# Optimization experiments

Hardware: AMD Instinct MI355X
Metric: run time of the kernel (lower is better)

Reference implementation:

```python
import jax, jax.numpy as jnp
import numpy as np

N_PATCHES = 14
HIDDEN_D = 768
N_HEADS = 12
D_HEAD = HIDDEN_D // N_HEADS
SEQ = N_PATCHES ** 2 + 1  # 197
INPUT_D = 3 * 16 * 16  # c * patch_h * patch_w = 768
LN_EPS = 1e-5


def positional_embeddings(seq_len, d):
    # result[i, j] = sin(i / 10000**(j/d)) if j even else cos(i / 10000**((j-1)/d))
    i = jnp.arange(seq_len, dtype=jnp.float32)[:, None]
    j = jnp.arange(d, dtype=jnp.float32)[None, :]
    even = (jnp.arange(d) % 2 == 0)[None, :]
    denom_even = jnp.power(10000.0, j / d)
    denom_odd = jnp.power(10000.0, (j - 1.0) / d)
    return jnp.where(even, jnp.sin(i / denom_even), jnp.cos(i / denom_odd))


def setup_inputs() -> dict:
    key = jax.random.key(0)
    ks = jax.random.split(key, 12)
    s = 0.02
    return {
        "images": jax.random.normal(ks[0], (128, 3, 224, 224), dtype=jnp.float32),
        "W_map": jax.random.normal(ks[1], (HIDDEN_D, INPUT_D), dtype=jnp.float32) * s,
        "b_map": jax.random.normal(ks[2], (HIDDEN_D,), dtype=jnp.float32) * s,
        "class_token": jax.random.uniform(ks[3], (1, HIDDEN_D), dtype=jnp.float32),
        "ln_w": jnp.ones((SEQ, HIDDEN_D), dtype=jnp.float32),
        "ln_b": jnp.zeros((SEQ, HIDDEN_D), dtype=jnp.float32),
        "Wq": jax.random.normal(ks[4], (N_HEADS, D_HEAD, D_HEAD), dtype=jnp.float32) * s,
        "bq": jax.random.normal(ks[5], (N_HEADS, D_HEAD), dtype=jnp.float32) * s,
        "Wk": jax.random.normal(ks[6], (N_HEADS, D_HEAD, D_HEAD), dtype=jnp.float32) * s,
        "bk": jax.random.normal(ks[7], (N_HEADS, D_HEAD), dtype=jnp.float32) * s,
        "Wv": jax.random.normal(ks[8], (N_HEADS, D_HEAD, D_HEAD), dtype=jnp.float32) * s,
        "bv": jax.random.normal(ks[9], (N_HEADS, D_HEAD), dtype=jnp.float32) * s,
    }


def _forward(images, W_map, b_map, class_token, ln_w, ln_b, Wq, bq, Wk, bk, Wv, bv):
    n = images.shape[0]
    # naive patchify (faithful to source: a plain reshape)
    patches = images.reshape(n, N_PATCHES ** 2, INPUT_D)
    # linear mapper: x @ W.T + b
    tokens = jnp.einsum("npi,di->npd", patches, W_map) + b_map
    # prepend class token
    cls = jnp.broadcast_to(class_token[None], (n, 1, HIDDEN_D))
    tokens = jnp.concatenate([cls, tokens], axis=1)  # [n, SEQ, D]
    # positional embeddings
    tokens = tokens + positional_embeddings(SEQ, HIDDEN_D)[None]
    # LayerNorm over last two dims (SEQ, D) jointly
    mean = jnp.mean(tokens, axis=(-2, -1), keepdims=True)
    var = jnp.var(tokens, axis=(-2, -1), keepdims=True)
    x = (tokens - mean) / jnp.sqrt(var + LN_EPS) * ln_w + ln_b
    # multi-head self-attention (batched over samples and heads)
    xh = x.reshape(n, SEQ, N_HEADS, D_HEAD)  # head-sliced channels
    q = jnp.einsum("bshd,hed->bshe", xh, Wq) + bq[None, None]
    k = jnp.einsum("bshd,hed->bshe", xh, Wk) + bk[None, None]
    v = jnp.einsum("bshd,hed->bshe", xh, Wv) + bv[None, None]
    att = jax.nn.softmax(
        jnp.einsum("bshd,bthd->bhst", q, k) / jnp.sqrt(jnp.float32(D_HEAD)), axis=-1
    )
    msa = jnp.einsum("bhst,bthd->bshd", att, v).reshape(n, SEQ, HIDDEN_D)
    return tokens + msa


def reference(images, W_map, b_map, class_token, ln_w, ln_b, Wq, bq, Wk, bk, Wv, bv):
    return _forward(images, W_map, b_map, class_token, ln_w, ln_b, Wq, bq, Wk, bk, Wv, bv)
```

## Files before the change

kernel.cpp:

```cpp
#include <hip/hip_runtime.h>

typedef float fx4 __attribute__((ext_vector_type(4)));
typedef __bf16 bf16x8 __attribute__((ext_vector_type(8)));
typedef unsigned short ushort8 __attribute__((ext_vector_type(8)));
typedef unsigned int uint2v __attribute__((ext_vector_type(2)));
typedef unsigned int uint4v __attribute__((ext_vector_type(4)));

#define MFMA16(a, b, c) __builtin_amdgcn_mfma_f32_16x16x32_bf16((a), (b), (c), 0, 0, 0)

#if __has_builtin(__builtin_amdgcn_exp2f)
#define EXP2(x) __builtin_amdgcn_exp2f(x)
#else
#define EXP2(x) exp2f(x)
#endif

__device__ __forceinline__ unsigned short f2bf(float f) {
  return __builtin_bit_cast(unsigned short, (__bf16)f);
}

__device__ __forceinline__ ushort8 pack8(fx4 a, fx4 b) {
  ushort8 v;
  v[0] = f2bf(a[0]); v[1] = f2bf(a[1]); v[2] = f2bf(a[2]); v[3] = f2bf(a[3]);
  v[4] = f2bf(b[0]); v[5] = f2bf(b[1]); v[6] = f2bf(b[2]); v[7] = f2bf(b[3]);
  return v;
}

__device__ __forceinline__ uint2v pack2(fx4 v) {
  uint2v r;
  r[0] = (unsigned int)f2bf(v[0]) | ((unsigned int)f2bf(v[1]) << 16);
  r[1] = (unsigned int)f2bf(v[2]) | ((unsigned int)f2bf(v[3]) << 16);
  return r;
}

__device__ __forceinline__ bf16x8 xfrm(uint2v A, uint2v B, int quad, int src0, int src1) {
  uint4v pf;
#pragma unroll
  for (int d = 0; d < 2; d++) {
    int a0 = __shfl((int)A[d], src0, 64);
    int b0 = __shfl((int)B[d], src0, 64);
    pf[d] = (unsigned int)((quad < 2) ? a0 : b0);
    int a1 = __shfl((int)A[d], src1, 64);
    int b1 = __shfl((int)B[d], src1, 64);
    pf[2 + d] = (unsigned int)((quad < 2) ? a1 : b1);
  }
  return __builtin_bit_cast(bf16x8, pf);
}

__device__ __forceinline__ void gl2lds16(const unsigned short* g, void* lds_base) {
  __builtin_amdgcn_global_load_lds(
      (const __attribute__((address_space(1))) void*)(unsigned long long)(g),
      (__attribute__((address_space(3))) void*)(unsigned int)(unsigned long long)(lds_base),
      16, 0, 0);
}

__global__ __launch_bounds__(256) void k_prep(
    const float* __restrict__ img, const float* __restrict__ W,
    const float* __restrict__ Wq, const float* __restrict__ Wk, const float* __restrict__ Wv,
    const float* __restrict__ ct,
    float* __restrict__ pe, unsigned short* __restrict__ imgbf, unsigned short* __restrict__ wbf,
    unsigned short* __restrict__ wqkv,
    float* __restrict__ out, float* __restrict__ sums, float* __restrict__ sqs) {
  const int bid = blockIdx.x, tid = threadIdx.x;
  if (bid < 591) {
    int idx = bid * 256 + tid;
    int s = idx / 768;
    int j = idx - s * 768;
    int jj = j & ~1;
    float ang = (float)s * expf((float)jj * (-9.210340371976184f / 768.0f));
    pe[idx] = (j & 1) ? cosf(ang) : sinf(ang);
  } else if (bid < 10287) {
    size_t i = ((size_t)(bid - 591) * 256 + tid) * 8;
    const float* src;
    unsigned short* dst;
    if (i < 19267584) { src = img + i; dst = imgbf + i; }
    else { size_t j = i - 19267584; src = W + j; dst = wbf + j; }
    const fx4* p = (const fx4*)src;
    *(ushort8*)dst = pack8(p[0], p[1]);
  } else if (bid < 10359) {
    int i = ((bid - 10287) * 256 + tid) * 8;
    const float* src = (i < 49152) ? (Wq + i) : (i < 98304 ? Wk + (i - 49152) : Wv + (i - 98304));
    const fx4* p = (const fx4*)src;
    *(ushort8*)(wqkv + i) = pack8(p[0], p[1]);
  } else {
    const int b = bid - 10359;
    float s = 0.f, q = 0.f;
#pragma unroll
    for (int it = 0; it < 3; it++) {
      int j = tid + it * 256;
      float v = ct[j] + ((j & 1) ? 1.f : 0.f);
      out[(size_t)b * 197 * 768 + j] = v;
      s += v; q += v * v;
    }
    for (int off = 32; off > 0; off >>= 1) { s += __shfl_down(s, off); q += __shfl_down(q, off); }
    __shared__ float rs[4], rq[4];
    int w = tid >> 6;
    if ((tid & 63) == 0) { rs[w] = s; rq[w] = q; }
    __syncthreads();
    if (tid == 0) {
      sums[b] = rs[0] + rs[1] + rs[2] + rs[3];
      sqs[b] = rq[0] + rq[1] + rq[2] + rq[3];
    }
  }
}

__global__ __launch_bounds__(256) void k_tokens(
    const unsigned short* __restrict__ imgbf, const unsigned short* __restrict__ wbf,
    const float* __restrict__ bmap, const float* __restrict__ pe,
    float* __restrict__ out, float* __restrict__ sums, float* __restrict__ sqs) {
  __shared__ __align__(16) ushort8 Sf[16 * 64];
  const int tid = threadIdx.x;
  const int idx = (blockIdx.x & 7) * 147 + (blockIdx.x >> 3);
  const int m0 = (idx / 6) * 128;
  const int n0 = (idx % 6) * 128;
  const int lane = tid & 63;
  const int w = tid >> 6;
  const int quad = lane >> 4, l16 = lane & 15;
  const int m_off = (w & 1) * 64, n_off = (w >> 1) * 64;

  fx4 acc[4][4];
#pragma unroll
  for (int i = 0; i < 4; i++)
#pragma unroll
    for (int j = 0; j < 4; j++) acc[i][j] = (fx4){0.f, 0.f, 0.f, 0.f};

  const unsigned short* pA = imgbf + (size_t)(m0 + w * 16 + l16) * 768 + quad * 8;
  const unsigned short* pB = wbf + (size_t)(n0 + w * 16 + l16) * 768 + quad * 8;
  void* lA0 = (void*)&Sf[(w) * 64];
  void* lA1 = (void*)&Sf[(4 + w) * 64];
  void* lB0 = (void*)&Sf[(8 + w) * 64];
  void* lB1 = (void*)&Sf[(12 + w) * 64];

  for (int k0 = 0; k0 < 768; k0 += 32) {
    __syncthreads();
    gl2lds16(pA + k0, lA0);
    gl2lds16(pA + 64 * 768 + k0, lA1);
    gl2lds16(pB + k0, lB0);
    gl2lds16(pB + 64 * 768 + k0, lB1);
    __syncthreads();
    bf16x8 a[4], b[4];
#pragma unroll
    for (int mt = 0; mt < 4; mt++)
      a[mt] = __builtin_bit_cast(bf16x8, Sf[((w & 1) * 4 + mt) * 64 + lane]);
#pragma unroll
    for (int nt = 0; nt < 4; nt++)
      b[nt] = __builtin_bit_cast(bf16x8, Sf[(8 + (w >> 1) * 4 + nt) * 64 + lane]);
#pragma unroll
    for (int mt = 0; mt < 4; mt++)
#pragma unroll
      for (int nt = 0; nt < 4; nt++) acc[mt][nt] = MFMA16(a[mt], b[nt], acc[mt][nt]);
  }

  float s0 = 0.f, q0 = 0.f, s1 = 0.f, q1 = 0.f;
  const int b0 = m0 / 196;
#pragma unroll
  for (int mt = 0; mt < 4; mt++) {
#pragma unroll
    for (int nt = 0; nt < 4; nt++) {
      const int col = n0 + n_off + nt * 16 + l16;
      const float bc = bmap[col];
#pragma unroll
      for (int r = 0; r < 4; r++) {
        const int gm = m0 + m_off + mt * 16 + quad * 4 + r;
        const int bb = gm / 196;
        const int ss = gm - bb * 196 + 1;
        float val = acc[mt][nt][r] + bc + pe[ss * 768 + col];
        out[((size_t)bb * 197 + ss) * 768 + col] = val;
        if (bb == b0) { s0 += val; q0 += val * val; }
        else          { s1 += val; q1 += val * val; }
      }
    }
  }
  for (int off = 32; off > 0; off >>= 1) {
    s0 += __shfl_down(s0, off); q0 += __shfl_down(q0, off);
    s1 += __shfl_down(s1, off); q1 += __shfl_down(q1, off);
  }
  if (lane == 0) {
    atomicAdd(&sums[b0], s0);
    atomicAdd(&sqs[b0], q0);
    if (b0 + 1 < 128) { atomicAdd(&sums[b0 + 1], s1); atomicAdd(&sqs[b0 + 1], q1); }
  }
}

__global__ __launch_bounds__(256, 3) void k_fused(
    const float* tok, const float* __restrict__ sums, const float* __restrict__ sqs,
    const float* __restrict__ lnw, const float* __restrict__ lnb,
    const unsigned short* __restrict__ wqkv,
    const float* __restrict__ bq, const float* __restrict__ bk, const float* __restrict__ bv,
    float* out) {
  __shared__ __align__(16) ushort8 Kf[26 * 64];
  __shared__ __align__(16) ushort8 Vf[24 * 64];
  __shared__ __align__(16) ushort8 Vt[4 * 32];
  const int tid = threadIdx.x;
  const int bh = blockIdx.x;
  const int b = bh / 12;
  const int h = bh - b * 12;
  const int lane = tid & 63;
  const int w = tid >> 6;
  const int quad = lane >> 4;
  const int l16 = lane & 15;
  const int src0 = l16 + ((quad & 1) << 5);
  const int src1 = src0 + 16;
  const float invN = 1.0f / 151296.0f;
  const float mean = sums[b] * invN;
  const float rstd = rsqrtf(sqs[b] * invN - mean * mean + 1e-5f);
  const int hcol = h * 64;

  bf16x8 qfr[4][2];

  bf16x8 wq[4][2], wk[4][2], wv[4][2];
#pragma unroll
  for (int et = 0; et < 4; et++) {
    const int ro = (et * 16 + l16) * 64 + quad * 8;
#pragma unroll
    for (int kk = 0; kk < 2; kk++) {
      wq[et][kk] = *(const bf16x8*)(wqkv + hcol * 64 + ro + kk * 32);
      wk[et][kk] = *(const bf16x8*)(wqkv + 49152 + hcol * 64 + ro + kk * 32);
      wv[et][kk] = *(const bf16x8*)(wqkv + 98304 + hcol * 64 + ro + kk * 32);
    }
  }

#pragma unroll
  for (int pi = 0; pi < 2; pi++) {
    const int jp = w + 4 * pi;
    if (jp <= 6) {
      bf16x8 xf[2][2];
#pragma unroll
      for (int s2 = 0; s2 < 2; s2++) {
        const int tt = 2 * jp + s2;
        if (tt < 13) {
          int ss = tt * 16 + l16;
          ss = (ss < 197) ? ss : 196;
#pragma unroll
          for (int kk = 0; kk < 2; kk++) {
            const int col = hcol + kk * 32 + quad * 8;
            const fx4* px = (const fx4*)(tok + (size_t)(b * 197 + ss) * 768 + col);
            const fx4* pw = (const fx4*)(lnw + (size_t)ss * 768 + col);
            const fx4* pb = (const fx4*)(lnb + (size_t)ss * 768 + col);
            fx4 y0 = (px[0] - mean) * rstd * pw[0] + pb[0];
            fx4 y1 = (px[1] - mean) * rstd * pw[1] + pb[1];
            xf[s2][kk] = __builtin_bit_cast(bf16x8, pack8(y0, y1));
          }
          fx4 aq[4], ak[4];
#pragma unroll
          for (int et = 0; et < 4; et++) {
            aq[et] = (fx4){0.f, 0.f, 0.f, 0.f};
            ak[et] = (fx4){0.f, 0.f, 0.f, 0.f};
          }
#pragma unroll
          for (int kk = 0; kk < 2; kk++)
#pragma unroll
            for (int et = 0; et < 4; et++) {
              aq[et] = MFMA16(wq[et][kk], xf[s2][kk], aq[et]);
              ak[et] = MFMA16(wk[et][kk], xf[s2][kk], ak[et]);
            }
          uint2v qp[4], kp[4];
#pragma unroll
          for (int et = 0; et < 4; et++) {
            fx4 bqv = *(const fx4*)(bq + hcol + et * 16 + quad * 4);
            fx4 bkv = *(const fx4*)(bk + hcol + et * 16 + quad * 4);
            qp[et] = pack2((aq[et] + bqv) * 0.18033688f);
            kp[et] = pack2(ak[et] + bkv);
          }
          const int qi = pi * 2 + s2;
#pragma unroll
          for (int kk = 0; kk < 2; kk++) {
            qfr[qi][kk] = xfrm(qp[2 * kk], qp[2 * kk + 1], quad, src0, src1);
            bf16x8 kfrag = xfrm(kp[2 * kk], kp[2 * kk + 1], quad, src0, src1);
            Kf[(tt * 2 + kk) * 64 + lane] = __builtin_bit_cast(ushort8, kfrag);
          }
        }
      }
      fx4 av[2][4];
#pragma unroll
      for (int s2 = 0; s2 < 2; s2++)
#pragma unroll
        for (int et = 0; et < 4; et++) av[s2][et] = (fx4){0.f, 0.f, 0.f, 0.f};
#pragma unroll
      for (int s2 = 0; s2 < 2; s2++) {
        const int tt = 2 * jp + s2;
        if (tt < 13) {
#pragma unroll
          for (int kk = 0; kk < 2; kk++)
#pragma unroll
            for (int et = 0; et < 4; et++)
              av[s2][et] = MFMA16(xf[s2][kk], wv[et][kk], av[s2][et]);
        }
      }
#pragma unroll
      for (int et = 0; et < 4; et++) {
        const float bvv = bv[hcol + et * 16 + l16];
        fx4 bb4 = (fx4){bvv, bvv, bvv, bvv};
        uint2v v0 = pack2(av[0][et] + bb4);
        uint2v v1 = pack2(av[1][et] + bb4);
        bf16x8 vfrag = xfrm(v0, v1, quad, src0, src1);
        if (jp < 6) Vf[(et * 6 + jp) * 64 + lane] = __builtin_bit_cast(ushort8, vfrag);
        else if (quad < 2) Vt[et * 32 + lane] = __builtin_bit_cast(ushort8, vfrag);
      }
    }
  }
  __syncthreads();

#pragma unroll
  for (int qi = 0; qi < 4; qi++) {
    const int mt = 2 * w + (qi >> 1) * 8 + (qi & 1);
    if (mt < 13) {
      fx4 sacc[13];
#pragma unroll
      for (int nt = 0; nt < 13; nt++) sacc[nt] = (fx4){0.f, 0.f, 0.f, 0.f};
#pragma unroll
      for (int kk = 0; kk < 2; kk++) {
        bf16x8 qf = qfr[qi][kk];
#pragma unroll
        for (int nt = 0; nt < 13; nt++) {
          bf16x8 kf = __builtin_bit_cast(bf16x8, Kf[(nt * 2 + kk) * 64 + lane]);
          sacc[nt] = MFMA16(kf, qf, sacc[nt]);
        }
      }
      float sm = 0.f;
      uint2v pk[13];
#pragma unroll
      for (int nt = 0; nt < 13; nt++) {
        fx4 p;
#pragma unroll
        for (int r = 0; r < 4; r++) {
          const bool valid = (nt < 12) | (quad * 4 + r < 5);
          p[r] = valid ? EXP2(sacc[nt][r]) : 0.f;
          sm += p[r];
        }
        pk[nt] = pack2(p);
      }
      sm += __shfl_xor(sm, 16);
      sm += __shfl_xor(sm, 32);
      const float inv = 1.0f / sm;

      fx4 oacc[4];
#pragma unroll
      for (int et = 0; et < 4; et++) oacc[et] = (fx4){0.f, 0.f, 0.f, 0.f};
#pragma unroll
      for (int kk = 0; kk < 7; kk++) {
        uint4v pf;
        if (kk < 6) {
          const int nA = 2 * kk, nB = 2 * kk + 1;
#pragma unroll
          for (int d = 0; d < 2; d++) {
            int a0 = __shfl((int)pk[nA][d], src0, 64);
            int b0 = __shfl((int)pk[nB][d], src0, 64);
            pf[d] = (unsigned int)((quad < 2) ? a0 : b0);
            int a1 = __shfl((int)pk[nA][d], src1, 64);
            int b1 = __shfl((int)pk[nB][d], src1, 64);
            pf[2 + d] = (unsigned int)((quad < 2) ? a1 : b1);
          }
        } else {
#pragma unroll
          for (int d = 0; d < 2; d++) {
            int a0 = __shfl((int)pk[12][d], src0, 64);
            pf[d] = (quad < 2) ? (unsigned int)a0 : 0u;
            int a1 = __shfl((int)pk[12][d], src1, 64);
            pf[2 + d] = (quad < 2) ? (unsigned int)a1 : 0u;
          }
        }
        bf16x8 pfrag = __builtin_bit_cast(bf16x8, pf);
#pragma unroll
        for (int et = 0; et < 4; et++) {
          bf16x8 vf;
          if (kk < 6) {
            vf = __builtin_bit_cast(bf16x8, Vf[(et * 6 + kk) * 64 + lane]);
          } else if (quad < 2) {
            vf = __builtin_bit_cast(bf16x8, Vt[et * 32 + lane]);
          } else {
            ushort8 z = {0, 0, 0, 0, 0, 0, 0, 0};
            vf = __builtin_bit_cast(bf16x8, z);
          }
          oacc[et] = MFMA16(vf, pfrag, oacc[et]);
        }
      }
      const int sg = mt * 16 + l16;
      if (sg < 197) {
        float* op = out + ((size_t)b * 197 + sg) * 768 + hcol + quad * 4;
#pragma unroll
        for (int et = 0; et < 4; et++) {
          fx4 cur = *(const fx4*)(op + et * 16);
          cur += oacc[et] * inv;
          *(fx4*)(op + et * 16) = cur;
        }
      }
    }
  }
}

extern "C" void kernel_launch(void* const* d_in, const int* in_sizes, int n_in,
                              void* d_out, int out_size, void* d_ws, size_t ws_size,
                              hipStream_t stream) {
  (void)in_sizes; (void)n_in; (void)out_size; (void)ws_size;
  const float* img  = (const float*)d_in[0];
  const float* Wmap = (const float*)d_in[1];
  const float* bmap = (const float*)d_in[2];
  const float* ct   = (const float*)d_in[3];
  const float* lnw  = (const float*)d_in[4];
  const float* lnb  = (const float*)d_in[5];
  const float* Wq   = (const float*)d_in[6];
  const float* bq   = (const float*)d_in[7];
  const float* Wk   = (const float*)d_in[8];
  const float* bk   = (const float*)d_in[9];
  const float* Wv   = (const float*)d_in[10];
  const float* bv   = (const float*)d_in[11];
  float* out = (float*)d_out;

  float* pe   = (float*)d_ws;
  float* sums = pe + 151296;
  float* sqs  = sums + 128;
  unsigned short* wbf   = (unsigned short*)(sqs + 128);
  unsigned short* imgbf = wbf + 589824;
  unsigned short* wqkv  = imgbf + (size_t)19267584;

  k_prep<<<10487, 256, 0, stream>>>(img, Wmap, Wq, Wk, Wv, ct,
                                    pe, imgbf, wbf, wqkv, out, sums, sqs);
  k_tokens<<<1176, 256, 0, stream>>>(imgbf, wbf, bmap, pe, out, sums, sqs);
  k_fused<<<1536, 256, 0, stream>>>(out, sums, sqs, lnw, lnb, wqkv, bq, bk, bv, out);
}
```

Measured before the change: 355.8 us.

## Process two query tiles per wave jointly in attention, prefetch residual, lower occupancy

Restructures the attention loop so each wave handles two query tiles together, sharing each K and V LDS fragment read across two MFMAs and interleaving independent MFMA chains. The residual tokens are loaded from global memory before the PV MFMA loop so the load latency overlaps compute, and s_setprio raises wave priority around the MFMA sections. Launch bounds drop from 3 to 2 waves per SIMD to give room for the doubled accumulator register footprint, at the cost of lower occupancy.

```diff
diff --git a/kernel.cpp b/kernel.cpp
--- a/kernel.cpp
+++ b/kernel.cpp
@@ -181,7 +181,7 @@
   }
 }
 
-__global__ __launch_bounds__(256, 3) void k_fused(
+__global__ __launch_bounds__(256, 2) void k_fused(
     const float* tok, const float* __restrict__ sums, const float* __restrict__ sqs,
     const float* __restrict__ lnw, const float* __restrict__ lnb,
     const unsigned short* __restrict__ wqkv,
@@ -206,6 +206,13 @@
   const int hcol = h * 64;
 
   bf16x8 qfr[4][2];
+  {
+    ushort8 z8 = {0, 0, 0, 0, 0, 0, 0, 0};
+#pragma unroll
+    for (int qi = 0; qi < 4; qi++)
+#pragma unroll
+      for (int kk = 0; kk < 2; kk++) qfr[qi][kk] = __builtin_bit_cast(bf16x8, z8);
+  }
 
   bf16x8 wq[4][2], wk[4][2], wv[4][2];
 #pragma unroll
@@ -301,65 +308,105 @@
   __syncthreads();
 
 #pragma unroll
-  for (int qi = 0; qi < 4; qi++) {
-    const int mt = 2 * w + (qi >> 1) * 8 + (qi & 1);
-    if (mt < 13) {
-      fx4 sacc[13];
-#pragma unroll
-      for (int nt = 0; nt < 13; nt++) sacc[nt] = (fx4){0.f, 0.f, 0.f, 0.f};
+  for (int pr = 0; pr < 2; pr++) {
+    const int mtA = 2 * w + pr * 8;
+    const int mtB = mtA + 1;
+    if (mtA < 13) {
+      const bool bval = (mtB < 13);
+      fx4 sA[13], sB[13];
+#pragma unroll
+      for (int nt = 0; nt < 13; nt++) {
+        sA[nt] = (fx4){0.f, 0.f, 0.f, 0.f};
+        sB[nt] = (fx4){0.f, 0.f, 0.f, 0.f};
+      }
+      __builtin_amdgcn_s_setprio(1);
 #pragma unroll
       for (int kk = 0; kk < 2; kk++) {
-        bf16x8 qf = qfr[qi][kk];
+        bf16x8 qa = qfr[pr * 2][kk];
+        bf16x8 qb = qfr[pr * 2 + 1][kk];
 #pragma unroll
         for (int nt = 0; nt < 13; nt++) {
           bf16x8 kf = __builtin_bit_cast(bf16x8, Kf[(nt * 2 + kk) * 64 + lane]);
-          sacc[nt] = MFMA16(kf, qf, sacc[nt]);
-        }
-      }
-      float sm = 0.f;
-      uint2v pk[13];
+          sA[nt] = MFMA16(kf, qa, sA[nt]);
+          sB[nt] = MFMA16(kf, qb, sB[nt]);
+        }
+      }
+      __builtin_amdgcn_s_setprio(0);
+
+      float smA = 0.f, smB = 0.f;
+      uint2v pkA[13], pkB[13];
 #pragma unroll
       for (int nt = 0; nt < 13; nt++) {
-        fx4 p;
+        fx4 pA, pB;
 #pragma unroll
         for (int r = 0; r < 4; r++) {
           const bool valid = (nt < 12) | (quad * 4 + r < 5);
-          p[r] = valid ? EXP2(sacc[nt][r]) : 0.f;
-          sm += p[r];
-        }
-        pk[nt] = pack2(p);
-      }
-      sm += __shfl_xor(sm, 16);
-      sm += __shfl_xor(sm, 32);
-      const float inv = 1.0f / sm;
-
-      fx4 oacc[4];
-#pragma unroll
-      for (int et = 0; et < 4; et++) oacc[et] = (fx4){0.f, 0.f, 0.f, 0.f};
+          pA[r] = valid ? EXP2(sA[nt][r]) : 0.f;
+          pB[r] = (valid && bval) ? EXP2(sB[nt][r]) : 0.f;
+          smA += pA[r];
+          smB += pB[r];
+        }
+        pkA[nt] = pack2(pA);
+        pkB[nt] = pack2(pB);
+      }
+      smA += __shfl_xor(smA, 16); smA += __shfl_xor(smA, 32);
+      smB += __shfl_xor(smB, 16); smB += __shfl_xor(smB, 32);
+      const float invA = 1.0f / smA;
+      const float invB = bval ? 1.0f / smB : 0.f;
+
+      const int sgA = mtA * 16 + l16;
+      const int sgB = mtB * 16 + l16;
+      float* opA = out + ((size_t)b * 197 + (sgA < 197 ? sgA : 196)) * 768 + hcol + quad * 4;
+      float* opB = out + ((size_t)b * 197 + (sgB < 197 ? sgB : 196)) * 768 + hcol + quad * 4;
+      fx4 curA[4], curB[4];
+#pragma unroll
+      for (int et = 0; et < 4; et++) {
+        curA[et] = *(const fx4*)(opA + et * 16);
+        curB[et] = *(const fx4*)(opB + et * 16);
+      }
+
+      fx4 oA[4], oB[4];
+#pragma unroll
+      for (int et = 0; et < 4; et++) {
+        oA[et] = (fx4){0.f, 0.f, 0.f, 0.f};
+        oB[et] = (fx4){0.f, 0.f, 0.f, 0.f};
+      }
+      __builtin_amdgcn_s_setprio(1);
 #pragma unroll
       for (int kk = 0; kk < 7; kk++) {
-        uint4v pf;
+        uint4v pfA, pfB;
         if (kk < 6) {
           const int nA = 2 * kk, nB = 2 * kk + 1;
 #pragma unroll
           for (int d = 0; d < 2; d++) {
-            int a0 = __shfl((int)pk[nA][d], src0, 64);
-            int b0 = __shfl((int)pk[nB][d], src0, 64);
-            pf[d] = (unsigned int)((quad < 2) ? a0 : b0);
-            int a1 = __shfl((int)pk[nA][d], src1, 64);
-            int b1 = __shfl((int)pk[nB][d], src1, 64);
-            pf[2 + d] = (unsigned int)((quad < 2) ? a1 : b1);
+            int a0 = __shfl((int)pkA[nA][d], src0, 64);
+            int b0 = __shfl((int)pkA[nB][d], src0, 64);
+            pfA[d] = (unsigned int)((quad < 2) ? a0 : b0);
+            int a1 = __shfl((int)pkA[nA][d], src1, 64);
+            int b1 = __shfl((int)pkA[nB][d], src1, 64);
+            pfA[2 + d] = (unsigned int)((quad < 2) ? a1 : b1);
+            int c0 = __shfl((int)pkB[nA][d], src0, 64);
+            int e0 = __shfl((int)pkB[nB][d], src0, 64);
+            pfB[d] = (unsigned int)((quad < 2) ? c0 : e0);
+            int c1 = __shfl((int)pkB[nA][d], src1, 64);
+            int e1 = __shfl((int)pkB[nB][d], src1, 64);
+            pfB[2 + d] = (unsigned int)((quad < 2) ? c1 : e1);
           }
         } else {
 #pragma unroll
           for (int d = 0; d < 2; d++) {
-            int a0 = __shfl((int)pk[12][d], src0, 64);
-            pf[d] = (quad < 2) ? (unsigned int)a0 : 0u;
-            int a1 = __shfl((int)pk[12][d], src1, 64);
-            pf[2 + d] = (quad < 2) ? (unsigned int)a1 : 0u;
-          }
-        }
-        bf16x8 pfrag = __builtin_bit_cast(bf16x8, pf);
+            int a0 = __shfl((int)pkA[12][d], src0, 64);
+            pfA[d] = (quad < 2) ? (unsigned int)a0 : 0u;
+            int a1 = __shfl((int)pkA[12][d], src1, 64);
+            pfA[2 + d] = (quad < 2) ? (unsigned int)a1 : 0u;
+            int c0 = __shfl((int)pkB[12][d], src0, 64);
+            pfB[d] = (quad < 2) ? (unsigned int)c0 : 0u;
+            int c1 = __shfl((int)pkB[12][d], src1, 64);
+            pfB[2 + d] = (quad < 2) ? (unsigned int)c1 : 0u;
+          }
+        }
+        bf16x8 fa = __builtin_bit_cast(bf16x8, pfA);
+        bf16x8 fb = __builtin_bit_cast(bf16x8, pfB);
 #pragma unroll
         for (int et = 0; et < 4; et++) {
           bf16x8 vf;
@@ -371,18 +418,19 @@
             ushort8 z = {0, 0, 0, 0, 0, 0, 0, 0};
             vf = __builtin_bit_cast(bf16x8, z);
           }
-          oacc[et] = MFMA16(vf, pfrag, oacc[et]);
-        }
-      }
-      const int sg = mt * 16 + l16;
-      if (sg < 197) {
-        float* op = out + ((size_t)b * 197 + sg) * 768 + hcol + quad * 4;
-#pragma unroll
-        for (int et = 0; et < 4; et++) {
-          fx4 cur = *(const fx4*)(op + et * 16);
-          cur += oacc[et] * inv;
-          *(fx4*)(op + et * 16) = cur;
-        }
+          oA[et] = MFMA16(vf, fa, oA[et]);
+          oB[et] = MFMA16(vf, fb, oB[et]);
+        }
+      }
+      __builtin_amdgcn_s_setprio(0);
+
+      if (sgA < 197) {
+#pragma unroll
+        for (int et = 0; et < 4; et++) *(fx4*)(opA + et * 16) = curA[et] + oA[et] * invA;
+      }
+      if (bval && sgB < 197) {
+#pragma unroll
+        for (int et = 0; et < 4; et++) *(fx4*)(opB + et * 16) = curB[et] + oB[et] * invB;
       }
     }
   }
```

After: 338.1 us. 5.0% less time.
